# Kernel tuning notes

Hardware: AMD Instinct MI355X
Metric: run time of the kernel (lower is better)

## Reference

```python
import jax, jax.numpy as jnp
import numpy as np
import math

H = 64
W = 64
POS_DIM = 64          # (enc_out*9) // patch_length**2
PL = 3                # patch_length
RPL = 3               # reference_patch_length -> 36 offsets
CENTER = (PL * PL) // 2  # 4
NOFF = (2 * RPL) ** 2    # 36


def _unfold3(feat):
    # torch F.unfold(feat, 3, padding=1).view(B, C*9, H, W): channel-major, then 3x3 kernel offsets
    B, C, h, w = feat.shape
    p = jnp.pad(feat, ((0, 0), (0, 0), (1, 1), (1, 1)))
    shifts = [p[:, :, i:i + h, j:j + w] for i in range(3) for j in range(3)]
    return jnp.stack(shifts, axis=2).reshape(B, C * 9, h, w)


def _sinu(rel_pair):
    # pos_enc_sinu_2d_for_point, vectorized: rel_pair [..., 2] -> [..., POS_DIM]
    half = POS_DIM // 2
    div = jnp.exp(jnp.arange(0.0, half, 2.0) * (-(math.log(10000.0) / half)))  # [half/2]
    a = rel_pair[..., 0:1] * div   # [..., half/2]
    b = rel_pair[..., 1:2] * div
    pa = jnp.stack([jnp.sin(a), jnp.cos(a)], axis=-1).reshape(*a.shape[:-1], half)  # interleaved sin/cos
    pb = jnp.stack([jnp.sin(b), jnp.cos(b)], axis=-1).reshape(*b.shape[:-1], half)
    return jnp.concatenate([pa, pb], axis=-1)


def _mlp(x, ws, bs):
    n = len(ws)
    for i in range(n):
        x = x @ ws[i] + bs[i]
        if i < n - 1:
            x = jax.nn.relu(x)
    return x


def _forward(inp, coord, cell, enc_w, enc_b, w0, b0, w1, b1, w2, b2, w3, b3, w4, b4):
    # encoder: 3x3 conv, stride 1, same padding
    feat = jax.lax.conv_general_dilated(inp, enc_w, (1, 1), 'SAME',
                                        dimension_numbers=('NCHW', 'OIHW', 'NCHW'))
    feat = feat + enc_b[None, :, None, None]
    feat = _unfold3(feat)  # [B, C*9, H, W]
    B, Cf, h, w = feat.shape
    Q = coord.shape[1]
    D = coord.shape[-1]  # 18
    rx = 1.0 / h  # 2/h/2
    ry = 1.0 / w
    eps = 1e-6

    offs = jnp.array([v for v in range(-RPL, RPL + 1) if v != 0], jnp.float32)  # [6]
    vx = jnp.repeat(offs, offs.shape[0])  # outer loop over vx -> [36]
    vy = jnp.tile(offs, offs.shape[0])
    even = (jnp.arange(D) % 2 == 0)
    shift = jnp.where(even[None, :], vx[:, None] * rx, vy[:, None] * ry) + eps  # [36, D]

    coord_ = coord[None] + shift[:, None, None, :]  # [36,B,Q,D]
    cc = jnp.clip(coord_[..., 2 * CENTER:2 * CENTER + 2], -1 + 1e-6, 1 - 1e-6)  # center coord [36,B,Q,2]
    # nearest grid_sample, align_corners=False: unnormalize then round
    iy = jnp.clip(jnp.round(((cc[..., 0] + 1) * h - 1) / 2), 0, h - 1).astype(jnp.int32)
    ix = jnp.clip(jnp.round(((cc[..., 1] + 1) * w - 1) / 2), 0, w - 1).astype(jnp.int32)

    flat = feat.transpose(0, 2, 3, 1).reshape(B, h * w, Cf)  # [B,HW,Cf]
    lin = iy * w + ix  # [36,B,Q]
    q_feat = flat[jnp.arange(B)[None, :, None], lin]  # [36,B,Q,Cf]

    # feat_coord at nearest pixel (make_coord cell centers)
    q_coord = jnp.stack([-1.0 + (2.0 * iy.astype(coord.dtype) + 1.0) / h,
                         -1.0 + (2.0 * ix.astype(coord.dtype) + 1.0) / w], axis=-1)  # [36,B,Q,2]

    rel = coord[None] - jnp.tile(q_coord, (1, 1, 1, PL * PL))  # [36,B,Q,18]
    # faithful to source: even indices scaled by h THEN by w; odd indices untouched
    scale = jnp.where(even, float(h) * float(w), 1.0)
    rel = rel * scale

    sinu = _sinu(rel.reshape(NOFF, B, Q, PL * PL, 2)).reshape(NOFF, B, Q, PL * PL * POS_DIM)
    x = q_feat + sinu

    rel_cell = cell * jnp.array([float(h), float(w)], dtype=cell.dtype)  # [B,Q,2]
    x = jnp.concatenate([x, jnp.broadcast_to(rel_cell[None], (NOFF,) + cell.shape)], axis=-1)

    pred = _mlp(x, [w0, w1, w2, w3, w4], [b0, b1, b2, b3, b4])  # [36,B,Q,27]

    area = jnp.abs(rel[..., 0] * rel[..., 1]) + 1e-9  # [36,B,Q]
    tot = area.sum(axis=0)
    perm = np.arange(NOFF)
    perm[[0, 1, 2, 3]] = [3, 2, 1, 0]  # local_ensemble area swap
    area = area[perm]
    return (pred * (area / tot)[..., None]).sum(axis=0)  # [B,Q,27]


def setup_inputs() -> dict:
    key = jax.random.key(0)
    ks = jax.random.split(key, 16)
    B, Q = 2, 2048
    inp = jax.random.normal(ks[0], (B, 3, H, W), jnp.float32)
    coord = jax.random.uniform(ks[1], (B, Q, PL * PL * 2), jnp.float32, minval=-1.0, maxval=1.0)
    cell = jnp.full((B, Q, 2), 2.0 / 192.0, jnp.float32)
    enc_w = jax.random.normal(ks[2], (64, 3, 3, 3), jnp.float32) * 0.05
    enc_b = jnp.zeros((64,), jnp.float32)
    dims = [578, 256, 256, 256, 256, 27]
    params = {}
    for i in range(5):
        fi, fo = dims[i], dims[i + 1]
        s = 1.0 / np.sqrt(fi)
        params['w%d' % i] = jax.random.uniform(ks[3 + 2 * i], (fi, fo), jnp.float32, minval=-s, maxval=s)
        params['b%d' % i] = jax.random.uniform(ks[4 + 2 * i], (fo,), jnp.float32, minval=-s, maxval=s)
    return dict(inp=inp, coord=coord, cell=cell, enc_w=enc_w, enc_b=enc_b, **params)


def reference(inp, coord, cell, enc_w, enc_b, w0, b0, w1, b1, w2, b2, w3, b3, w4, b4):
    return _forward(inp, coord, cell, enc_w, enc_b, w0, b0, w1, b1, w2, b2, w3, b3, w4, b4)
```

## Files before the change

### kernel.cpp

```cpp
#include <hip/hip_runtime.h>
#include <math.h>

typedef _Float16 f16;
typedef f16 f16x8 __attribute__((ext_vector_type(8)));
typedef f16 f16x2 __attribute__((ext_vector_type(2)));
typedef float f32x4 __attribute__((ext_vector_type(4)));

#define BB 2
#define QQ 2048
#define CF 576
#define NOFF 36
#define NBQ (BB*QQ)
#define NROWS (NOFF*NBQ)
#define FEAT_ELEMS (BB*66*66*64)
#define MROWS 48
#define NWG (NROWS/MROWS)
#define PITCHB 512

__global__ __launch_bounds__(256) void k_conv(const float* __restrict__ inp,
                                              const float* __restrict__ ew,
                                              const float* __restrict__ eb,
                                              f16* __restrict__ feat) {
    int idx = blockIdx.x * 256 + threadIdx.x;
    if (idx >= FEAT_ELEMS) return;
    int c = idx & 63;
    int t = idx >> 6;
    int x = t % 66; t /= 66;
    int y = t % 66;
    int b = t / 66;
    float v = 0.f;
    if (y >= 1 && y <= 64 && x >= 1 && x <= 64) {
        int yr = y - 1, xr = x - 1;
        v = eb[c];
        #pragma unroll
        for (int i = 0; i < 3; ++i)
            #pragma unroll
            for (int ky = 0; ky < 3; ++ky) {
                int yy = yr + ky - 1;
                if (yy < 0 || yy > 63) continue;
                #pragma unroll
                for (int kx = 0; kx < 3; ++kx) {
                    int xx = xr + kx - 1;
                    if (xx < 0 || xx > 63) continue;
                    v = fmaf(inp[((b*3 + i)*64 + yy)*64 + xx],
                             ew[((c*3 + i)*3 + ky)*3 + kx], v);
                }
            }
    }
    feat[idx] = (f16)v;
}

__global__ __launch_bounds__(256) void k_wcvt(const float* __restrict__ w0,
                                              const float* __restrict__ w1,
                                              const float* __restrict__ w2,
                                              const float* __restrict__ w3,
                                              const float* __restrict__ w4,
                                              f16* __restrict__ wt0, f16* __restrict__ wt1,
                                              f16* __restrict__ wt2, f16* __restrict__ wt3,
                                              f16* __restrict__ wt4) {
    int i = blockIdx.x * 256 + threadIdx.x;
    if (i < 19*256*32) {
        int kk = i & 31, col = (i >> 5) & 255, ks = i >> 13;
        int k = ks*32 + kk;
        wt0[i] = (f16)((k < 578) ? w0[k*256 + col] : 0.f);
        return;
    }
    i -= 19*256*32;
    if (i < 3*65536) {
        int l = i >> 16, j = i & 65535;
        int kk = j & 31, col = (j >> 5) & 255, ks = j >> 13;
        int k = ks*32 + kk;
        const float* w = (l == 0) ? w1 : (l == 1) ? w2 : w3;
        f16* wt = (l == 0) ? wt1 : (l == 1) ? wt2 : wt3;
        wt[j] = (f16)w[k*256 + col];
        return;
    }
    i -= 3*65536;
    if (i < 8192) {
        int kk = i & 31, col = (i >> 5) & 31, ks = i >> 10;
        int k = ks*32 + kk;
        wt4[i] = (f16)((col < 27) ? w4[k*27 + col] : 0.f);
    }
}

__global__ __launch_bounds__(256) void k_prep(const float* __restrict__ coord,
                                              float* __restrict__ qc0w,
                                              float* __restrict__ qc1w,
                                              float* __restrict__ areaw,
                                              int* __restrict__ iposw) {
    int R = blockIdx.x * 256 + threadIdx.x;
    if (R >= NROWS) return;
    int bq = R / 36, n = R - bq*36;
    const float offs[6] = {-3.f, -2.f, -1.f, 1.f, 2.f, 3.f};
    float vx = offs[n / 6];
    float vy = offs[n % 6];
    const float* cp = coord + bq * 18;
    float cc0 = cp[8] + vx * (1.0f/64.0f) + 1e-6f;
    float cc1 = cp[9] + vy * (1.0f/64.0f) + 1e-6f;
    cc0 = fminf(fmaxf(cc0, -1.f + 1e-6f), 1.f - 1e-6f);
    cc1 = fminf(fmaxf(cc1, -1.f + 1e-6f), 1.f - 1e-6f);
    int iy = (int)rintf(((cc0 + 1.f) * 64.f - 1.f) * 0.5f);
    int ix = (int)rintf(((cc1 + 1.f) * 64.f - 1.f) * 0.5f);
    iy = min(max(iy, 0), 63);
    ix = min(max(ix, 0), 63);
    float qc0 = -1.f + (2.f * (float)iy + 1.f) * (1.0f/64.0f);
    float qc1 = -1.f + (2.f * (float)ix + 1.f) * (1.0f/64.0f);
    float rel0 = (cp[0] - qc0) * 4096.f;
    float rel1 = (cp[1] - qc1);
    qc0w[R] = qc0;
    qc1w[R] = qc1;
    areaw[R] = fabsf(rel0 * rel1) + 1e-9f;
    int b = bq >> 11;
    iposw[R] = ((b*66 + iy)*66 + ix) * 64;
}

__global__ __launch_bounds__(256) void k_wgt(const float* __restrict__ areaw,
                                             float* __restrict__ wgtw) {
    int bq = blockIdx.x * 256 + threadIdx.x;
    if (bq >= NBQ) return;
    float a[36];
    float tot = 0.f;
    #pragma unroll
    for (int n = 0; n < 36; ++n) { a[n] = areaw[bq*36 + n]; tot += a[n]; }
    #pragma unroll
    for (int n = 0; n < 36; ++n) {
        int pn = (n < 4) ? 3 - n : n;
        wgtw[bq*36 + n] = a[pn] / tot;
    }
}

template <int COLS2, int JOFF>
__device__ __forceinline__ void buildX(f16* sX, const f16* __restrict__ feat,
                                       const int* s_ipos, const float* s_crd,
                                       const float* s_qc0, const float* s_qc1,
                                       const float* s_cx, const float* s_cy,
                                       const float* s_div, int tid) {
    constexpr int NPAIR = MROWS * COLS2;
    #pragma unroll 2
    for (int p = tid; p < NPAIR; p += 512) {
        int r = p / COLS2;
        int j = JOFF + ((p - r * COLS2) << 1);
        float v0, v1;
        if (j < CF) {
            int c0 = j / 9,  s0 = j  - c0*9;
            int j1 = j + 1;
            int c1 = j1 / 9, s1 = j1 - c1*9;
            int ip = s_ipos[r];
            float f0 = (float)feat[ip + ((s0/3)*66 + (s0 - (s0/3)*3))*64 + c0];
            float f1 = (float)feat[ip + ((s1/3)*66 + (s1 - (s1/3)*3))*64 + c1];
            int d  = j & 63;
            int pl = j >> 6;
            int h2 = d >> 5;
            float qc = h2 ? s_qc1[r] : s_qc0[r];
            float sc = h2 ? 1.f : 4096.f;
            float comp = (s_crd[r*18 + 2*pl + h2] - qc) * sc;
            float arg  = comp * s_div[(d & 31) >> 1];
            float rev = arg * 0.15915494309189535f;
            rev = rev - rintf(rev);
            v0 = f0 + __builtin_amdgcn_sinf(rev);
            v1 = f1 + __builtin_amdgcn_cosf(rev);
        } else if (j == CF) {
            v0 = s_cx[r]; v1 = s_cy[r];
        } else {
            v0 = 0.f; v1 = 0.f;
        }
        uint off = (uint)(r*PITCHB + (j - JOFF)*2);
        off ^= (uint)((r & 7) << 4);
        f16x2 hv = { (f16)v0, (f16)v1 };
        *(f16x2*)((char*)sX + off) = hv;
    }
}

template <int NKS, int NNT, int PITCHC>
__device__ __forceinline__ void gemmT(const f16* sX, const f16* __restrict__ Wt,
                                      int colbase, int lg,
                                      const uint (&abase)[3], uint aswz,
                                      f32x4 (&acc)[3][NNT]) {
    #pragma unroll
    for (int ks = 0; ks < NKS; ++ks) {
        f16x8 a[3], b[NNT];
        #pragma unroll
        for (int nt = 0; nt < NNT; ++nt)
            b[nt] = *(const f16x8*)(Wt + (ks*PITCHC + colbase + nt*16)*32 + lg*8);
        #pragma unroll
        for (int mt = 0; mt < 3; ++mt)
            a[mt] = *(const f16x8*)((const char*)sX + ((abase[mt] + (uint)(ks*64)) ^ aswz));
        #pragma unroll
        for (int mt = 0; mt < 3; ++mt)
            #pragma unroll
            for (int nt = 0; nt < NNT; ++nt)
                acc[mt][nt] = __builtin_amdgcn_mfma_f32_16x16x32_f16(a[mt], b[nt], acc[mt][nt], 0, 0, 0);
    }
}

__device__ __forceinline__ void waitv4() {
    asm volatile("s_waitcnt vmcnt(4)" ::: "memory");
    __builtin_amdgcn_sched_barrier(0);
}
__device__ __forceinline__ void waitv0() {
    asm volatile("s_waitcnt vmcnt(0)" ::: "memory");
    __builtin_amdgcn_sched_barrier(0);
}
__device__ __forceinline__ void waitlgkm() {
    asm volatile("s_waitcnt lgkmcnt(0)" ::: "memory");
    __builtin_amdgcn_sched_barrier(0);
}
__device__ __forceinline__ void barrier() {
    __builtin_amdgcn_s_barrier();
    __builtin_amdgcn_sched_barrier(0);
}

__global__ __launch_bounds__(512, 2) void k_mlp(
    const float* __restrict__ coord, const float* __restrict__ cellp,
    const f16* __restrict__ feat,
    const float* __restrict__ qc0w, const float* __restrict__ qc1w,
    const float* __restrict__ wgtw, const int* __restrict__ iposw,
    const f16* __restrict__ wt0, const f16* __restrict__ wt1,
    const f16* __restrict__ wt2, const f16* __restrict__ wt3,
    const f16* __restrict__ wt4,
    const float* __restrict__ b0, const float* __restrict__ b1,
    const float* __restrict__ b2, const float* __restrict__ b3,
    const float* __restrict__ b4,
    float* __restrict__ partial)
{
    __shared__ f16 sX[MROWS * 256];
    __shared__ f16 sBB[3][8192];
    __shared__ float s_crd[MROWS * 18];
    __shared__ float s_qc0[MROWS], s_qc1[MROWS], s_cx[MROWS], s_cy[MROWS], s_wgt[MROWS];
    __shared__ int   s_ipos[MROWS];
    __shared__ float s_div[16];

    int tid = threadIdx.x;
    int R0  = blockIdx.x * MROWS;

    if (tid < 16) s_div[tid] = expf((float)(2*tid) * -0.28782313662425575f);
    if (tid < MROWS) {
        int R  = R0 + tid;
        int bq = R / 36;
        s_qc0[tid]  = __builtin_nontemporal_load(&qc0w[R]);
        s_qc1[tid]  = __builtin_nontemporal_load(&qc1w[R]);
        s_wgt[tid]  = __builtin_nontemporal_load(&wgtw[R]);
        s_ipos[tid] = __builtin_nontemporal_load(&iposw[R]);
        s_cx[tid]   = cellp[bq*2 + 0] * 64.f;
        s_cy[tid]   = cellp[bq*2 + 1] * 64.f;
    }
    for (int i = tid; i < MROWS*18; i += 512) {
        int r = i / 18, d = i - r*18;
        s_crd[i] = coord[((R0 + r)/36)*18 + d];
    }

    int lane = tid & 63;
    int wc   = tid >> 6;
    int l15  = lane & 15;
    int lg   = lane >> 4;
    uint aswz = (uint)((lane & 7) << 4);

    uint abase[3];
    #pragma unroll
    for (int mt = 0; mt < 3; ++mt) {
        int row = mt*16 + l15;
        abase[mt] = (uint)(row * PITCHB + lg*16);
    }

    float bvL[4][2], bv4[2];
    {
        const float* Bs[4] = {b0, b1, b2, b3};
        #pragma unroll
        for (int L = 0; L < 4; ++L)
            #pragma unroll
            for (int nt = 0; nt < 2; ++nt) {
                bvL[L][nt] = Bs[L][wc*32 + nt*16 + l15];
                asm volatile("" :: "v"(bvL[L][nt]));
            }
        #pragma unroll
        for (int nt = 0; nt < 2; ++nt) {
            int col = nt*16 + l15;
            bv4[nt] = (col < 27) ? b4[col] : 0.f;
            asm volatile("" :: "v"(bv4[nt]));
        }
    }

    f32x4 acc[3][2];
    auto zacc = [&]() {
        #pragma unroll
        for (int mt = 0; mt < 3; ++mt)
            #pragma unroll
            for (int nt = 0; nt < 2; ++nt)
                #pragma unroll
                for (int i = 0; i < 4; ++i) acc[mt][nt][i] = 0.f;
    };

    auto stage = [&](f16* dst, const f16* __restrict__ Wt, int ks) {
        if (tid < 256) {
            const char* g = (const char*)Wt + (size_t)ks * 16384 + (size_t)tid * 64;
            char* d = (char*)dst + tid * 16;
            #pragma unroll
            for (int i = 0; i < 4; ++i) {
                __builtin_amdgcn_global_load_lds(
                    (const __attribute__((address_space(1))) void*)(g + i*16),
                    (__attribute__((address_space(3))) void*)(d + i*4096),
                    16, 0, 0);
            }
        }
        __builtin_amdgcn_sched_barrier(0);
    };

    auto computeK = [&](const f16* sB, int lks) {
        f16x8 a[3], b[2];
        #pragma unroll
        for (int nt = 0; nt < 2; ++nt)
            b[nt] = *(const f16x8*)((const char*)sB + lg*4096 + (wc*32 + nt*16 + l15)*16);
        #pragma unroll
        for (int mt = 0; mt < 3; ++mt)
            a[mt] = *(const f16x8*)((const char*)sX + ((abase[mt] + (uint)(lks*64)) ^ aswz));
        #pragma unroll
        for (int mt = 0; mt < 3; ++mt)
            #pragma unroll
            for (int nt = 0; nt < 2; ++nt)
                acc[mt][nt] = __builtin_amdgcn_mfma_f32_16x16x32_f16(a[mt], b[nt], acc[mt][nt], 0, 0, 0);
    };

    auto epi = [&](const float (&bv)[2]) {
        #pragma unroll
        for (int nt = 0; nt < 2; ++nt) {
            int col = wc*32 + nt*16 + l15;
            #pragma unroll
            for (int mt = 0; mt < 3; ++mt)
                #pragma unroll
                for (int i = 0; i < 4; ++i) {
                    int row = mt*16 + lg*4 + i;
                    float v = fmaxf(acc[mt][nt][i] + bv[nt], 0.f);
                    uint off = (uint)(row*PITCHB + col*2) ^ (uint)((row & 7) << 4);
                    *(f16*)((char*)sX + off) = (f16)v;
                }
        }
    };

    __syncthreads();

    zacc();
    buildX<128, 0>(sX, feat, s_ipos, s_crd, s_qc0, s_qc1, s_cx, s_cy, s_div, tid);
    stage(sBB[0], wt0, 0);
    stage(sBB[1], wt0, 1);
    waitlgkm(); barrier();
    #pragma unroll
    for (int ks = 0; ks < 8; ++ks) {
        waitv4();
        barrier();
        stage(sBB[(ks + 2) % 3], wt0, ks + 2);
        computeK(sBB[ks % 3], ks);
    }
    barrier();
    buildX<128, 256>(sX, feat, s_ipos, s_crd, s_qc0, s_qc1, s_cx, s_cy, s_div, tid);
    waitlgkm(); barrier();
    #pragma unroll
    for (int t = 0; t < 8; ++t) {
        int ks = t + 8;
        waitv4();
        barrier();
        stage(sBB[(ks + 2) % 3], wt0, ks + 2);
        computeK(sBB[ks % 3], t);
    }
    barrier();
    buildX<48, 512>(sX, feat, s_ipos, s_crd, s_qc0, s_qc1, s_cx, s_cy, s_div, tid);
    waitlgkm(); barrier();
    #pragma unroll
    for (int t = 0; t < 3; ++t) {
        int ks = t + 16;
        if (ks + 1 < 19) waitv4(); else waitv0();
        barrier();
        if (ks + 2 < 19) stage(sBB[(ks + 2) % 3], wt0, ks + 2);
        computeK(sBB[ks % 3], t);
    }

    const f16* Ws[3] = {wt1, wt2, wt3};
    #pragma unroll
    for (int L = 0; L < 3; ++L) {
        barrier();
        stage(sBB[0], Ws[L], 0);
        stage(sBB[1], Ws[L], 1);
        epi(bvL[L]);
        zacc();
        waitlgkm(); barrier();
        #pragma unroll
        for (int ks = 0; ks < 8; ++ks) {
            if (ks + 1 < 8) waitv4(); else waitv0();
            barrier();
            if (ks + 2 < 8) stage(sBB[(ks + 2) % 3], Ws[L], ks + 2);
            computeK(sBB[ks % 3], ks);
        }
    }
    barrier();
    epi(bvL[3]);
    waitlgkm(); barrier();

    if (wc == 0) {
        f32x4 a4[3][2];
        #pragma unroll
        for (int mt = 0; mt < 3; ++mt)
            #pragma unroll
            for (int nt = 0; nt < 2; ++nt)
                #pragma unroll
                for (int i = 0; i < 4; ++i) a4[mt][nt][i] = 0.f;
        gemmT<8,2,32>(sX, wt4, l15, lg, abase, aswz, a4);
        int split = 36 - (R0 % 36);
        #pragma unroll
        for (int nt = 0; nt < 2; ++nt) {
            int col = nt*16 + l15;
            float s0 = 0.f, s1 = 0.f;
            #pragma unroll
            for (int mt = 0; mt < 3; ++mt)
                #pragma unroll
                for (int i = 0; i < 4; ++i) {
                    int row = mt*16 + lg*4 + i;
                    float v = (a4[mt][nt][i] + bv4[nt]) * s_wgt[row];
                    if (row < split) s0 += v; else s1 += v;
                }
            s0 += __shfl_xor(s0, 16, 64);
            s0 += __shfl_xor(s0, 32, 64);
            s1 += __shfl_xor(s1, 16, 64);
            s1 += __shfl_xor(s1, 32, 64);
            if (lg == 0 && col < 27) {
                __builtin_nontemporal_store(s0, &partial[(size_t)blockIdx.x*56 + col]);
                __builtin_nontemporal_store(s1, &partial[(size_t)blockIdx.x*56 + 28 + col]);
            }
        }
    }
}

__global__ __launch_bounds__(256) void k_red(const float* __restrict__ partial,
                                             float* __restrict__ out) {
    int i = blockIdx.x * 256 + threadIdx.x;
    if (i >= NBQ * 27) return;
    int bq = i / 27, col = i - bq*27;
    int r_lo = bq * 36;
    int w0 = r_lo / 48, w1 = (r_lo + 35) / 48;
    float s = 0.f;
    for (int w = w0; w <= w1; ++w) {
        int seg = (bq == (w*48)/36) ? 0 : 1;
        s += __builtin_nontemporal_load(&partial[(size_t)w*56 + seg*28 + col]);
    }
    out[i] = s;
}

extern "C" void kernel_launch(void* const* d_in, const int* in_sizes, int n_in,
                              void* d_out, int out_size, void* d_ws, size_t ws_size,
                              hipStream_t stream) {
    const float* inp   = (const float*)d_in[0];
    const float* coord = (const float*)d_in[1];
    const float* cellp = (const float*)d_in[2];
    const float* enc_w = (const float*)d_in[3];
    const float* enc_b = (const float*)d_in[4];
    const float* w0 = (const float*)d_in[5];
    const float* b0 = (const float*)d_in[6];
    const float* w1 = (const float*)d_in[7];
    const float* b1 = (const float*)d_in[8];
    const float* w2 = (const float*)d_in[9];
    const float* b2 = (const float*)d_in[10];
    const float* w3 = (const float*)d_in[11];
    const float* b3 = (const float*)d_in[12];
    const float* w4 = (const float*)d_in[13];
    const float* b4 = (const float*)d_in[14];
    float* outp = (float*)d_out;

    float* ws    = (float*)d_ws;
    f16*   feat  = (f16*)ws;
    float* qc0w  = (float*)(feat + FEAT_ELEMS);
    float* qc1w  = qc0w + NROWS;
    float* areaw = qc1w + NROWS;
    float* wgtw  = areaw + NROWS;
    int*   iposw = (int*)(wgtw + NROWS);
    float* partial = (float*)(iposw + NROWS);
    f16*   wt0   = (f16*)(partial + (size_t)NWG*56);
    f16*   wt1   = wt0 + 19*256*32;
    f16*   wt2   = wt1 + 65536;
    f16*   wt3   = wt2 + 65536;
    f16*   wt4   = wt3 + 65536;

    k_conv<<<(FEAT_ELEMS + 255)/256, 256, 0, stream>>>(inp, enc_w, enc_b, feat);
    k_wcvt<<<1408, 256, 0, stream>>>(w0, w1, w2, w3, w4, wt0, wt1, wt2, wt3, wt4);
    k_prep<<<NROWS/256, 256, 0, stream>>>(coord, qc0w, qc1w, areaw, iposw);
    k_wgt<<<(NBQ + 255)/256, 256, 0, stream>>>(areaw, wgtw);
    k_mlp<<<NWG, 512, 0, stream>>>(coord, cellp, feat, qc0w, qc1w, wgtw, iposw,
                                   wt0, wt1, wt2, wt3, wt4,
                                   b0, b1, b2, b3, b4, partial);
    k_red<<<(NBQ*27 + 255)/256, 256, 0, stream>>>(partial, outp);
}
```

Before: 288.9 us.

## Factor positional-encoding GEMM into per-axis precomputed partials; DMA feature gather into LDS

The positional-encoding part of layer 0 is split by linearity into an x-only and a y-only term. Each depends on just one of the 6 offset values per query, so a new kernel computes these 256-wide partial products once per (query, offset) and layer 0's epilogue adds them back. The main kernel now only multiplies the gathered unfold features, whose weight rows are permuted to a channel-contiguous order, and those features are loaded straight into LDS with global_load_lds. This removes per-row sin/cos work and most of the K dimension from the big GEMM, at the cost of an extra kernel, more workspace, and extra global reads of the partials in the epilogue.

```diff
diff --git a/kernel.cpp b/kernel.cpp
--- a/kernel.cpp
+++ b/kernel.cpp
@@ -8,10 +8,10 @@
 
 #define BB 2
 #define QQ 2048
-#define CF 576
 #define NOFF 36
 #define NBQ (BB*QQ)
 #define NROWS (NOFF*NBQ)
+#define NSE (NBQ*6)
 #define FEAT_ELEMS (BB*66*66*64)
 #define MROWS 48
 #define NWG (NROWS/MROWS)
@@ -57,12 +57,20 @@
                                               const float* __restrict__ w4,
                                               f16* __restrict__ wt0, f16* __restrict__ wt1,
                                               f16* __restrict__ wt2, f16* __restrict__ wt3,
-                                              f16* __restrict__ wt4) {
+                                              f16* __restrict__ wt4,
+                                              f16* __restrict__ w0x, f16* __restrict__ w0y) {
     int i = blockIdx.x * 256 + threadIdx.x;
     if (i < 19*256*32) {
         int kk = i & 31, col = (i >> 5) & 255, ks = i >> 13;
-        int k = ks*32 + kk;
-        wt0[i] = (f16)((k < 578) ? w0[k*256 + col] : 0.f);
+        int kp = ks*32 + kk;
+        float v = 0.f;
+        if (kp < 576) {
+            int j = (kp & 63)*9 + (kp >> 6);
+            v = w0[j*256 + col];
+        } else if (kp < 578) {
+            v = w0[kp*256 + col];
+        }
+        wt0[i] = (f16)v;
         return;
     }
     i -= 19*256*32;
@@ -80,12 +88,21 @@
         int kk = i & 31, col = (i >> 5) & 31, ks = i >> 10;
         int k = ks*32 + kk;
         wt4[i] = (f16)((col < 27) ? w4[k*27 + col] : 0.f);
+        return;
+    }
+    i -= 8192;
+    if (i < 2*9*256*32) {
+        int half = i / (9*256*32);
+        int j2 = i - half*(9*256*32);
+        int kk = j2 & 31, col = (j2 >> 5) & 255, ks = j2 >> 13;
+        int m = ks*32 + kk;
+        int j = (m >> 5)*64 + (m & 31) + (half ? 32 : 0);
+        f16* dst = half ? w0y : w0x;
+        dst[j2] = (f16)w0[j*256 + col];
     }
 }
 
 __global__ __launch_bounds__(256) void k_prep(const float* __restrict__ coord,
-                                              float* __restrict__ qc0w,
-                                              float* __restrict__ qc1w,
                                               float* __restrict__ areaw,
                                               int* __restrict__ iposw) {
     int R = blockIdx.x * 256 + threadIdx.x;
@@ -107,8 +124,6 @@
     float qc1 = -1.f + (2.f * (float)ix + 1.f) * (1.0f/64.0f);
     float rel0 = (cp[0] - qc0) * 4096.f;
     float rel1 = (cp[1] - qc1);
-    qc0w[R] = qc0;
-    qc1w[R] = qc1;
     areaw[R] = fabsf(rel0 * rel1) + 1e-9f;
     int b = bq >> 11;
     iposw[R] = ((b*66 + iy)*66 + ix) * 64;
@@ -129,50 +144,8 @@
     }
 }
 
-template <int COLS2, int JOFF>
-__device__ __forceinline__ void buildX(f16* sX, const f16* __restrict__ feat,
-                                       const int* s_ipos, const float* s_crd,
-                                       const float* s_qc0, const float* s_qc1,
-                                       const float* s_cx, const float* s_cy,
-                                       const float* s_div, int tid) {
-    constexpr int NPAIR = MROWS * COLS2;
-    #pragma unroll 2
-    for (int p = tid; p < NPAIR; p += 512) {
-        int r = p / COLS2;
-        int j = JOFF + ((p - r * COLS2) << 1);
-        float v0, v1;
-        if (j < CF) {
-            int c0 = j / 9,  s0 = j  - c0*9;
-            int j1 = j + 1;
-            int c1 = j1 / 9, s1 = j1 - c1*9;
-            int ip = s_ipos[r];
-            float f0 = (float)feat[ip + ((s0/3)*66 + (s0 - (s0/3)*3))*64 + c0];
-            float f1 = (float)feat[ip + ((s1/3)*66 + (s1 - (s1/3)*3))*64 + c1];
-            int d  = j & 63;
-            int pl = j >> 6;
-            int h2 = d >> 5;
-            float qc = h2 ? s_qc1[r] : s_qc0[r];
-            float sc = h2 ? 1.f : 4096.f;
-            float comp = (s_crd[r*18 + 2*pl + h2] - qc) * sc;
-            float arg  = comp * s_div[(d & 31) >> 1];
-            float rev = arg * 0.15915494309189535f;
-            rev = rev - rintf(rev);
-            v0 = f0 + __builtin_amdgcn_sinf(rev);
-            v1 = f1 + __builtin_amdgcn_cosf(rev);
-        } else if (j == CF) {
-            v0 = s_cx[r]; v1 = s_cy[r];
-        } else {
-            v0 = 0.f; v1 = 0.f;
-        }
-        uint off = (uint)(r*PITCHB + (j - JOFF)*2);
-        off ^= (uint)((r & 7) << 4);
-        f16x2 hv = { (f16)v0, (f16)v1 };
-        *(f16x2*)((char*)sX + off) = hv;
-    }
-}
-
 template <int NKS, int NNT, int PITCHC>
-__device__ __forceinline__ void gemmT(const f16* sX, const f16* __restrict__ Wt,
+__device__ __forceinline__ void gemmT(const f16* sA, const f16* __restrict__ Wt,
                                       int colbase, int lg,
                                       const uint (&abase)[3], uint aswz,
                                       f32x4 (&acc)[3][NNT]) {
@@ -184,12 +157,94 @@
             b[nt] = *(const f16x8*)(Wt + (ks*PITCHC + colbase + nt*16)*32 + lg*8);
         #pragma unroll
         for (int mt = 0; mt < 3; ++mt)
-            a[mt] = *(const f16x8*)((const char*)sX + ((abase[mt] + (uint)(ks*64)) ^ aswz));
+            a[mt] = *(const f16x8*)((const char*)sA + ((abase[mt] + (uint)(ks*64)) ^ aswz));
         #pragma unroll
         for (int mt = 0; mt < 3; ++mt)
             #pragma unroll
             for (int nt = 0; nt < NNT; ++nt)
                 acc[mt][nt] = __builtin_amdgcn_mfma_f32_16x16x32_f16(a[mt], b[nt], acc[mt][nt], 0, 0, 0);
+    }
+}
+
+__global__ __launch_bounds__(256) void k_seso(const float* __restrict__ coord,
+                                              const f16* __restrict__ w0x,
+                                              const f16* __restrict__ w0y,
+                                              f16* __restrict__ se, f16* __restrict__ so) {
+    __shared__ f16 sS[48 * 320];
+    __shared__ float s_cpx[48][9], s_cpy[48][9];
+    __shared__ float s_div[16];
+
+    int tid = threadIdx.x;
+    int R0  = blockIdx.x * 48;
+
+    if (tid < 16) s_div[tid] = expf((float)(2*tid) * -0.28782313662425575f);
+    if (tid < 48) {
+        int R = R0 + tid;
+        int bq = R / 6, vi = R - bq*6;
+        const float offs[6] = {-3.f, -2.f, -1.f, 1.f, 2.f, 3.f};
+        float v = offs[vi];
+        const float* cp = coord + bq * 18;
+        float cc0 = cp[8] + v * (1.0f/64.0f) + 1e-6f;
+        float cc1 = cp[9] + v * (1.0f/64.0f) + 1e-6f;
+        cc0 = fminf(fmaxf(cc0, -1.f + 1e-6f), 1.f - 1e-6f);
+        cc1 = fminf(fmaxf(cc1, -1.f + 1e-6f), 1.f - 1e-6f);
+        int iy = (int)rintf(((cc0 + 1.f) * 64.f - 1.f) * 0.5f);
+        int ix = (int)rintf(((cc1 + 1.f) * 64.f - 1.f) * 0.5f);
+        iy = min(max(iy, 0), 63);
+        ix = min(max(ix, 0), 63);
+        float qc0 = -1.f + (2.f * (float)iy + 1.f) * (1.0f/64.0f);
+        float qc1 = -1.f + (2.f * (float)ix + 1.f) * (1.0f/64.0f);
+        #pragma unroll
+        for (int pl = 0; pl < 9; ++pl) {
+            s_cpx[tid][pl] = (cp[2*pl]     - qc0) * 4096.f;
+            s_cpy[tid][pl] = (cp[2*pl + 1] - qc1);
+        }
+    }
+    __syncthreads();
+
+    int lane = tid & 63, wc = tid >> 6, l15 = lane & 15, lg = lane >> 4;
+    uint aswz = (uint)((lane & 7) << 4);
+    uint abase[3];
+    #pragma unroll
+    for (int mt = 0; mt < 3; ++mt)
+        abase[mt] = (uint)((mt*16 + l15) * 640 + lg*16);
+    int colbase = wc*64 + l15;
+
+    #pragma unroll
+    for (int half = 0; half < 2; ++half) {
+        for (int idx = tid; idx < 48*288; idx += 256) {
+            int r = idx / 288, m = idx - r*288;
+            int pl = m >> 5, d = m & 31, t = d >> 1;
+            float comp = half ? s_cpy[r][pl] : s_cpx[r][pl];
+            float arg = comp * s_div[t];
+            float rev = arg * 0.15915494309189535f;
+            rev = rev - rintf(rev);
+            float v = (d & 1) ? __builtin_amdgcn_cosf(rev) : __builtin_amdgcn_sinf(rev);
+            uint off = (uint)(r*640 + m*2) ^ (uint)((r & 7) << 4);
+            *(f16*)((char*)sS + off) = (f16)v;
+        }
+        __syncthreads();
+        f32x4 acc[3][4];
+        #pragma unroll
+        for (int mt = 0; mt < 3; ++mt)
+            #pragma unroll
+            for (int nt = 0; nt < 4; ++nt)
+                #pragma unroll
+                for (int i = 0; i < 4; ++i) acc[mt][nt][i] = 0.f;
+        gemmT<9,4,256>(sS, half ? w0y : w0x, colbase, lg, abase, aswz, acc);
+        f16* dst = half ? so : se;
+        #pragma unroll
+        for (int nt = 0; nt < 4; ++nt) {
+            int col = wc*64 + nt*16 + l15;
+            #pragma unroll
+            for (int mt = 0; mt < 3; ++mt)
+                #pragma unroll
+                for (int i = 0; i < 4; ++i) {
+                    int row = mt*16 + lg*4 + i;
+                    dst[(size_t)(R0 + row)*256 + col] = (f16)acc[mt][nt][i];
+                }
+        }
+        __syncthreads();
     }
 }
 
@@ -211,13 +266,13 @@
 }
 
 __global__ __launch_bounds__(512, 2) void k_mlp(
-    const float* __restrict__ coord, const float* __restrict__ cellp,
+    const float* __restrict__ cellp,
     const f16* __restrict__ feat,
-    const float* __restrict__ qc0w, const float* __restrict__ qc1w,
     const float* __restrict__ wgtw, const int* __restrict__ iposw,
     const f16* __restrict__ wt0, const f16* __restrict__ wt1,
     const f16* __restrict__ wt2, const f16* __restrict__ wt3,
     const f16* __restrict__ wt4,
+    const f16* __restrict__ se, const f16* __restrict__ so,
     const float* __restrict__ b0, const float* __restrict__ b1,
     const float* __restrict__ b2, const float* __restrict__ b3,
     const float* __restrict__ b4,
@@ -225,28 +280,21 @@
 {
     __shared__ f16 sX[MROWS * 256];
     __shared__ f16 sBB[3][8192];
-    __shared__ float s_crd[MROWS * 18];
-    __shared__ float s_qc0[MROWS], s_qc1[MROWS], s_cx[MROWS], s_cy[MROWS], s_wgt[MROWS];
-    __shared__ int   s_ipos[MROWS];
-    __shared__ float s_div[16];
+    __shared__ float s_cx[MROWS], s_cy[MROWS], s_wgt[MROWS];
+    __shared__ int   s_ipos[MROWS], s_sei[MROWS], s_soi[MROWS];
 
     int tid = threadIdx.x;
     int R0  = blockIdx.x * MROWS;
 
-    if (tid < 16) s_div[tid] = expf((float)(2*tid) * -0.28782313662425575f);
     if (tid < MROWS) {
         int R  = R0 + tid;
-        int bq = R / 36;
-        s_qc0[tid]  = __builtin_nontemporal_load(&qc0w[R]);
-        s_qc1[tid]  = __builtin_nontemporal_load(&qc1w[R]);
+        int bq = R / 36, n = R - bq*36;
         s_wgt[tid]  = __builtin_nontemporal_load(&wgtw[R]);
         s_ipos[tid] = __builtin_nontemporal_load(&iposw[R]);
         s_cx[tid]   = cellp[bq*2 + 0] * 64.f;
         s_cy[tid]   = cellp[bq*2 + 1] * 64.f;
-    }
-    for (int i = tid; i < MROWS*18; i += 512) {
-        int r = i / 18, d = i - r*18;
-        s_crd[i] = coord[((R0 + r)/36)*18 + d];
+        s_sei[tid]  = (bq*6 + n/6) * 256;
+        s_soi[tid]  = (bq*6 + n%6) * 256;
     }
 
     int lane = tid & 63;
@@ -255,11 +303,12 @@
     int lg   = lane >> 4;
     uint aswz = (uint)((lane & 7) << 4);
 
-    uint abase[3];
+    uint abase[3], abase2[3];
     #pragma unroll
     for (int mt = 0; mt < 3; ++mt) {
         int row = mt*16 + l15;
-        abase[mt] = (uint)(row * PITCHB + lg*16);
+        abase[mt]  = (uint)(row * PITCHB + lg*16);
+        abase2[mt] = (uint)(row * 256    + lg*16);
     }
 
     float bvL[4][2], bv4[2];
@@ -290,7 +339,7 @@
                 for (int i = 0; i < 4; ++i) acc[mt][nt][i] = 0.f;
     };
 
-    auto stage = [&](f16* dst, const f16* __restrict__ Wt, int ks) {
+    auto stageW = [&](f16* dst, const f16* __restrict__ Wt, int ks) {
         if (tid < 256) {
             const char* g = (const char*)Wt + (size_t)ks * 16384 + (size_t)tid * 64;
             char* d = (char*)dst + tid * 16;
@@ -305,6 +354,50 @@
         __builtin_amdgcn_sched_barrier(0);
     };
 
+    auto stageXc = [&](int phase) {
+        #pragma unroll
+        for (int i = 0; i < 3; ++i) {
+            int chunk = tid + i*512;
+            int r = chunk >> 5;
+            int w = (chunk & 31) << 4;
+            int wl = w ^ ((r & 7) << 4);
+            int jp = wl >> 1;
+            int s = phase*4 + (jp >> 6);
+            int c = jp & 63;
+            int doff = (s/3)*66 + (s - (s/3)*3);
+            const f16* src = feat + (s_ipos[r] + doff*64 + c);
+            __builtin_amdgcn_global_load_lds(
+                (const __attribute__((address_space(1))) void*)src,
+                (__attribute__((address_space(3))) void*)((char*)sX + chunk*16),
+                16, 0, 0);
+        }
+        __builtin_amdgcn_sched_barrier(0);
+    };
+
+    auto stageXc2 = [&]() {
+        #pragma unroll
+        for (int i = 0; i < 2; ++i) {
+            int chunk = tid + i*512;
+            if (chunk < 768) {
+                int r = chunk >> 4;
+                int w = (chunk & 15) << 4;
+                const f16* src;
+                int ip = s_ipos[r];
+                if (w < 128) {
+                    int wl = w ^ ((r & 7) << 4);
+                    src = feat + (ip + 134*64 + (wl >> 1));
+                } else {
+                    src = feat + ip;
+                }
+                __builtin_amdgcn_global_load_lds(
+                    (const __attribute__((address_space(1))) void*)src,
+                    (__attribute__((address_space(3))) void*)((char*)sX + chunk*16),
+                    16, 0, 0);
+            }
+        }
+        __builtin_amdgcn_sched_barrier(0);
+    };
+
     auto computeK = [&](const f16* sB, int lks) {
         f16x8 a[3], b[2];
         #pragma unroll
@@ -313,6 +406,20 @@
         #pragma unroll
         for (int mt = 0; mt < 3; ++mt)
             a[mt] = *(const f16x8*)((const char*)sX + ((abase[mt] + (uint)(lks*64)) ^ aswz));
+        #pragma unroll
+        for (int mt = 0; mt < 3; ++mt)
+            #pragma unroll
+            for (int nt = 0; nt < 2; ++nt)
+                acc[mt][nt] = __builtin_amdgcn_mfma_f32_16x16x32_f16(a[mt], b[nt], acc[mt][nt], 0, 0, 0);
+    };
+    auto computeK2 = [&](const f16* sB, int lks) {
+        f16x8 a[3], b[2];
+        #pragma unroll
+        for (int nt = 0; nt < 2; ++nt)
+            b[nt] = *(const f16x8*)((const char*)sB + lg*4096 + (wc*32 + nt*16 + l15)*16);
+        #pragma unroll
+        for (int mt = 0; mt < 3; ++mt)
+            a[mt] = *(const f16x8*)((const char*)sX + ((abase2[mt] + (uint)(lks*64)) ^ aswz));
         #pragma unroll
         for (int mt = 0; mt < 3; ++mt)
             #pragma unroll
@@ -335,62 +442,90 @@
                 }
         }
     };
+    auto epi0 = [&](const float (&bv)[2]) {
+        #pragma unroll
+        for (int mt = 0; mt < 3; ++mt)
+            #pragma unroll
+            for (int i = 0; i < 4; ++i) {
+                int row = mt*16 + lg*4 + i;
+                int sei = s_sei[row], soi = s_soi[row];
+                #pragma unroll
+                for (int nt = 0; nt < 2; ++nt) {
+                    int col = wc*32 + nt*16 + l15;
+                    float addv = (float)se[sei + col] + (float)so[soi + col];
+                    float v = fmaxf(acc[mt][nt][i] + addv + bv[nt], 0.f);
+                    uint off = (uint)(row*PITCHB + col*2) ^ (uint)((row & 7) << 4);
+                    *(f16*)((char*)sX + off) = (f16)v;
+                }
+            }
+    };
 
     __syncthreads();
 
     zacc();
-    buildX<128, 0>(sX, feat, s_ipos, s_crd, s_qc0, s_qc1, s_cx, s_cy, s_div, tid);
-    stage(sBB[0], wt0, 0);
-    stage(sBB[1], wt0, 1);
+    stageXc(0);
+    stageW(sBB[0], wt0, 0);
+    stageW(sBB[1], wt0, 1);
+    waitv4(); barrier();
+    #pragma unroll
+    for (int ks = 0; ks < 7; ++ks) {
+        stageW(sBB[(ks + 2) % 3], wt0, ks + 2);
+        computeK(sBB[ks % 3], ks);
+        waitv4(); barrier();
+    }
+    stageW(sBB[0], wt0, 9);
+    computeK(sBB[1], 7);
+    waitv4(); barrier();
+    stageXc(1);
+    waitv0(); barrier();
+    #pragma unroll
+    for (int ks = 8; ks < 15; ++ks) {
+        stageW(sBB[(ks + 2) % 3], wt0, ks + 2);
+        computeK(sBB[ks % 3], ks - 8);
+        waitv4(); barrier();
+    }
+    stageW(sBB[2], wt0, 17);
+    computeK(sBB[0], 7);
+    waitv4(); barrier();
+    stageXc2();
+    waitv0();
+    if (tid < 48) {
+        uint base = (uint)(tid * 256);
+        uint sw   = (uint)((tid & 7) << 4);
+        f16x2 cv = { (f16)s_cx[tid], (f16)s_cy[tid] };
+        *(f16x2*)((char*)sX + base + (128u ^ sw)) = cv;
+        f16x2 z = { (f16)0.f, (f16)0.f };
+        #pragma unroll
+        for (int q = 66; q < 96; q += 2)
+            *(f16x2*)((char*)sX + base + (((uint)(q*2)) ^ sw)) = z;
+    }
     waitlgkm(); barrier();
-    #pragma unroll
-    for (int ks = 0; ks < 8; ++ks) {
-        waitv4();
+    stageW(sBB[0], wt0, 18);
+    computeK2(sBB[1], 0);
+    computeK2(sBB[2], 1);
+    waitv0();
+    computeK2(sBB[0], 2);
+    barrier();
+
+    const f16* Ws[3] = {wt1, wt2, wt3};
+    #pragma unroll
+    for (int L = 0; L < 3; ++L) {
+        stageW(sBB[0], Ws[L], 0);
+        stageW(sBB[1], Ws[L], 1);
+        if (L == 0) epi0(bvL[0]); else epi(bvL[L]);
+        zacc();
+        waitv4(); waitlgkm(); barrier();
+        #pragma unroll
+        for (int ks = 0; ks < 6; ++ks) {
+            stageW(sBB[(ks + 2) % 3], Ws[L], ks + 2);
+            computeK(sBB[ks % 3], ks);
+            waitv4(); barrier();
+        }
+        computeK(sBB[0], 6);
+        waitv0(); barrier();
+        computeK(sBB[1], 7);
         barrier();
-        stage(sBB[(ks + 2) % 3], wt0, ks + 2);
-        computeK(sBB[ks % 3], ks);
-    }
-    barrier();
-    buildX<128, 256>(sX, feat, s_ipos, s_crd, s_qc0, s_qc1, s_cx, s_cy, s_div, tid);
-    waitlgkm(); barrier();
-    #pragma unroll
-    for (int t = 0; t < 8; ++t) {
-        int ks = t + 8;
-        waitv4();
-        barrier();
-        stage(sBB[(ks + 2) % 3], wt0, ks + 2);
-        computeK(sBB[ks % 3], t);
-    }
-    barrier();
-    buildX<48, 512>(sX, feat, s_ipos, s_crd, s_qc0, s_qc1, s_cx, s_cy, s_div, tid);
-    waitlgkm(); barrier();
-    #pragma unroll
-    for (int t = 0; t < 3; ++t) {
-        int ks = t + 16;
-        if (ks + 1 < 19) waitv4(); else waitv0();
-        barrier();
-        if (ks + 2 < 19) stage(sBB[(ks + 2) % 3], wt0, ks + 2);
-        computeK(sBB[ks % 3], t);
-    }
-
-    const f16* Ws[3] = {wt1, wt2, wt3};
-    #pragma unroll
-    for (int L = 0; L < 3; ++L) {
-        barrier();
-        stage(sBB[0], Ws[L], 0);
-        stage(sBB[1], Ws[L], 1);
-        epi(bvL[L]);
-        zacc();
-        waitlgkm(); barrier();
-        #pragma unroll
-        for (int ks = 0; ks < 8; ++ks) {
-            if (ks + 1 < 8) waitv4(); else waitv0();
-            barrier();
-            if (ks + 2 < 8) stage(sBB[(ks + 2) % 3], Ws[L], ks + 2);
-            computeK(sBB[ks % 3], ks);
-        }
-    }
-    barrier();
+    }
     epi(bvL[3]);
     waitlgkm(); barrier();
 
@@ -465,9 +600,7 @@
 
     float* ws    = (float*)d_ws;
     f16*   feat  = (f16*)ws;
-    float* qc0w  = (float*)(feat + FEAT_ELEMS);
-    float* qc1w  = qc0w + NROWS;
-    float* areaw = qc1w + NROWS;
+    float* areaw = (float*)(feat + FEAT_ELEMS);
     float* wgtw  = areaw + NROWS;
     int*   iposw = (int*)(wgtw + NROWS);
     float* partial = (float*)(iposw + NROWS);
@@ -476,13 +609,18 @@
     f16*   wt2   = wt1 + 65536;
     f16*   wt3   = wt2 + 65536;
     f16*   wt4   = wt3 + 65536;
+    f16*   w0x   = wt4 + 8192;
+    f16*   w0y   = w0x + 9*256*32;
+    f16*   sep   = w0y + 9*256*32;
+    f16*   sop   = sep + (size_t)NSE*256;
 
     k_conv<<<(FEAT_ELEMS + 255)/256, 256, 0, stream>>>(inp, enc_w, enc_b, feat);
-    k_wcvt<<<1408, 256, 0, stream>>>(w0, w1, w2, w3, w4, wt0, wt1, wt2, wt3, wt4);
-    k_prep<<<NROWS/256, 256, 0, stream>>>(coord, qc0w, qc1w, areaw, iposw);
+    k_wcvt<<<1984, 256, 0, stream>>>(w0, w1, w2, w3, w4, wt0, wt1, wt2, wt3, wt4, w0x, w0y);
+    k_prep<<<NROWS/256, 256, 0, stream>>>(coord, areaw, iposw);
     k_wgt<<<(NBQ + 255)/256, 256, 0, stream>>>(areaw, wgtw);
-    k_mlp<<<NWG, 512, 0, stream>>>(coord, cellp, feat, qc0w, qc1w, wgtw, iposw,
-                                   wt0, wt1, wt2, wt3, wt4,
+    k_seso<<<NSE/48, 256, 0, stream>>>(coord, w0x, w0y, sep, sop);
+    k_mlp<<<NWG, 512, 0, stream>>>(cellp, feat, wgtw, iposw,
+                                   wt0, wt1, wt2, wt3, wt4, sep, sop,
                                    b0, b1, b2, b3, b4, partial);
     k_red<<<(NBQ*27 + 255)/256, 256, 0, stream>>>(partial, outp);
 }
```

New measurement: 293.0 us. Within noise of the previous version (+1.4%).
